# Performance work log

Measured on AMD Instinct MI355X. Metric: run time of the kernel, lower is better.

Reference implementation:

```python
import jax, jax.numpy as jnp
import numpy as np

HEADS = 8
RATIO = 8
EPS = 1e-5


def conv3d(x, w, b, groups=1, pad=0):
    # x: [N,C,D,H,W], w: [O, C//groups, kd,kh,kw]
    out = jax.lax.conv_general_dilated(
        x, w, window_strides=(1, 1, 1),
        padding=[(pad, pad)] * 3,
        feature_group_count=groups,
        dimension_numbers=('NCDHW', 'OIDHW', 'NCDHW'))
    return out + b[None, :, None, None, None]


def setup_inputs() -> dict:
    key = jax.random.key(0)
    ks = jax.random.split(key, 8)
    n, C, t, h, w = 4, 512, 16, 28, 28
    Cm = C // RATIO           # 64
    Kc, Vc = 256, 256
    s = 0.05
    return {
        'x': jax.random.normal(ks[0], (n, C, t, h, w), jnp.float32),
        'pw1_w': jax.random.normal(ks[1], (Cm, C, 1, 1, 1), jnp.float32) * s,
        'pw1_b': jnp.zeros((Cm,), jnp.float32),
        'dw_w': jax.random.normal(ks[2], (Cm, 1, 3, 3, 3), jnp.float32) * s,
        'dw_b': jnp.zeros((Cm,), jnp.float32),
        'k_w': jax.random.normal(ks[3], (Kc, Cm, 1, 1, 1), jnp.float32) * s,
        'k_b': jnp.zeros((Kc,), jnp.float32),
        'q_w': jax.random.normal(ks[4], (Kc, Cm, 1, 1, 1), jnp.float32) * s,
        'q_b': jnp.zeros((Kc,), jnp.float32),
        'v_w': jax.random.normal(ks[5], (Vc, Cm, 1, 1, 1), jnp.float32) * s,
        'v_b': jnp.zeros((Vc,), jnp.float32),
        'rp_w': jax.random.normal(ks[6], (C, Vc, 1, 1, 1), jnp.float32) * s,
        'rp_b': jnp.zeros((C,), jnp.float32),
    }


def reference(x, pw1_w, pw1_b, dw_w, dw_b, k_w, k_b, q_w, q_b, v_w, v_b, rp_w, rp_b):
    n, C, t, h, w = x.shape
    N = t * h * w
    Cm = pw1_w.shape[0]
    Kc, Vc = k_w.shape[0], v_w.shape[0]
    hk, hv = Kc // HEADS, Vc // HEADS

    residual = x
    # DepthwiseConv: 1x1x1 pointwise then 3x3x3 depthwise
    mid = conv3d(x, pw1_w, pw1_b)
    mid = conv3d(mid, dw_w, dw_b, groups=Cm, pad=1)

    keys = conv3d(mid, k_w, k_b).reshape(n, HEADS, hk, N)
    queries = conv3d(mid, q_w, q_b).reshape(n, HEADS, hk, N)
    values = conv3d(mid, v_w, v_b).reshape(n, HEADS, hv, N)

    # linear attention: softmax keys over tokens, queries over head channels
    key = jax.nn.softmax(keys, axis=3)       # over N tokens
    query = jax.nn.softmax(queries, axis=2)  # over hk channels

    # context: [n, H, hk, hv]
    context = jnp.einsum('nhkt,nhvt->nhkv', key, values)
    # attended: [n, H, hv, N]
    attended = jnp.einsum('nhkv,nhkt->nhvt', context, query)
    aggregated = attended.reshape(n, Vc, t, h, w)

    out = conv3d(aggregated, rp_w, rp_b) + residual
    # f.layer_norm(x, x.size()): normalize over the ENTIRE tensor (all dims)
    mu = out.mean()
    var = out.var()
    return (out - mu) / jnp.sqrt(var + EPS)
```

## Files before the change

### kernel.cpp

```cpp
#include <hip/hip_runtime.h>
#include <hip/hip_bf16.h>
#include <math.h>

#define NB 4
#define S_TOK 12544
#define N_TOTAL 25690112ull
#define EPS 1e-5f

typedef short s16x8 __attribute__((ext_vector_type(8)));
typedef float f32x4 __attribute__((ext_vector_type(4)));

__device__ __forceinline__ short f2bf(float f) {
    unsigned u = __builtin_bit_cast(unsigned, f);
    u += 0x7fffu + ((u >> 16) & 1u);
    return (short)(u >> 16);
}

__global__ __launch_bounds__(256) void prep_k(
    const float* __restrict__ pw1_w, const float* __restrict__ k_w,
    const float* __restrict__ q_w, const float* __restrict__ rp_w,
    short* __restrict__ wb)
{
    int i = blockIdx.x * 256 + threadIdx.x;
#pragma unroll
    for (int r = 0; r < 4; ++r, i += 49152) {
        float v;
        if (i < 32768) v = pw1_w[i];
        else if (i < 49152) v = k_w[i - 32768];
        else if (i < 65536) v = q_w[i - 49152];
        else v = rp_w[i - 65536];
        wb[i] = f2bf(v);
    }
}

template<int NT, int WM, int WS, bool XTRANS, bool EPI>
__global__ __launch_bounds__(NT) void gemm_mfma(
    const short* __restrict__ Wb, const float* __restrict__ bias,
    const void* __restrict__ Xv, float* __restrict__ O,
    const float* __restrict__ R, float* __restrict__ stats,
    int M, int K, int S)
{
    constexpr int BM = WM * 64;
    constexpr int BS = WS * 64;
    __shared__ __align__(16) short Xt[BS][64];
    __shared__ __align__(16) short Wt[BM][64];

    const int tid  = threadIdx.x;
    const int lane = tid & 63;
    const int wave = tid >> 6;
    const int mb = blockIdx.x * BM;
    const int sb = blockIdx.y * BS;
    const size_t nb = blockIdx.z;

    const int wm0 = (wave / WS) * 64;
    const int ws0 = (wave % WS) * 64;

    f32x4 acc[4][4];
#pragma unroll
    for (int i = 0; i < 4; ++i)
#pragma unroll
        for (int j = 0; j < 4; ++j) acc[i][j] = (f32x4){0.f, 0.f, 0.f, 0.f};

    const int srow = tid >> 1;
    const int sb4  = (tid & 1) * 4;

    for (int k0 = 0; k0 < K; k0 += 64) {
        __syncthreads();
        {
            const short* wrow = Wb + (size_t)(mb + srow) * K + k0;
            const int sw = srow & 7;
#pragma unroll
            for (int b = 0; b < 4; ++b) {
                const int blk = sb4 + b;
                s16x8 v = *(const s16x8*)(wrow + (blk ^ sw) * 8);
                *(s16x8*)(&Wt[srow][blk * 8]) = v;
            }
        }
        if (XTRANS) {
            const int kr = tid & 63;
            constexpr int SPAN = (BS * 64) / NT;
            const int s0 = (tid >> 6) * SPAN;
            const float* xr = (const float*)Xv + nb * (size_t)K * S
                              + (size_t)(k0 + kr) * S + sb + s0;
            const int blo = (kr & 7) * 2;
            const int bhi = kr >> 3;
            char* base = (char*)Xt;
#pragma unroll
            for (int u = 0; u < SPAN / 4; ++u) {
                float4 v = *(const float4*)(xr + u * 4);
                const int s_ = s0 + u * 4;
                *(short*)(base + (s_ + 0) * 128 + ((bhi ^ ((s_ + 0) & 7)) << 4) + blo) = f2bf(v.x);
                *(short*)(base + (s_ + 1) * 128 + ((bhi ^ ((s_ + 1) & 7)) << 4) + blo) = f2bf(v.y);
                *(short*)(base + (s_ + 2) * 128 + ((bhi ^ ((s_ + 2) & 7)) << 4) + blo) = f2bf(v.z);
                *(short*)(base + (s_ + 3) * 128 + ((bhi ^ ((s_ + 3) & 7)) << 4) + blo) = f2bf(v.w);
            }
        } else {
            const short* xrow = (const short*)Xv + nb * (size_t)S * K
                                + (size_t)(sb + srow) * K + k0;
            const int sw = srow & 7;
#pragma unroll
            for (int b = 0; b < 4; ++b) {
                const int blk = sb4 + b;
                s16x8 v = *(const s16x8*)(xrow + (blk ^ sw) * 8);
                *(s16x8*)(&Xt[srow][blk * 8]) = v;
            }
        }
        __syncthreads();

#pragma unroll
        for (int kk = 0; kk < 2; ++kk) {
            s16x8 af[4], bg[4];
#pragma unroll
            for (int i = 0; i < 4; ++i) {
                const int row = ws0 + i * 16 + (lane & 15);
                const int blk = (kk * 4 + (lane >> 4)) ^ (row & 7);
                af[i] = *(const s16x8*)((const char*)Xt + row * 128 + blk * 16);
            }
#pragma unroll
            for (int j = 0; j < 4; ++j) {
                const int row = wm0 + j * 16 + (lane & 15);
                const int blk = (kk * 4 + (lane >> 4)) ^ (row & 7);
                bg[j] = *(const s16x8*)((const char*)Wt + row * 128 + blk * 16);
            }
#pragma unroll
            for (int i = 0; i < 4; ++i)
#pragma unroll
                for (int j = 0; j < 4; ++j)
                    acc[i][j] = __builtin_amdgcn_mfma_f32_16x16x32_bf16(
                        af[i], bg[j], acc[i][j], 0, 0, 0);
        }
    }

    float lsum = 0.f, lss = 0.f;
    const int chL = lane & 15, tq = (lane >> 4) * 4;
#pragma unroll
    for (int j = 0; j < 4; ++j) {
        const int ch = mb + wm0 + j * 16 + chL;
        const float bi = bias[ch];
        float* orow = O + nb * (size_t)M * S + (size_t)ch * S;
#pragma unroll
        for (int i = 0; i < 4; ++i) {
            const int t0 = sb + ws0 + i * 16 + tq;
            f32x4 a = acc[i][j];
            a.x += bi; a.y += bi; a.z += bi; a.w += bi;
            if (EPI) {
                const float4 r = *(const float4*)(R + nb * (size_t)M * S + (size_t)ch * S + t0);
                a.x += r.x; a.y += r.y; a.z += r.z; a.w += r.w;
                lsum += a.x + a.y + a.z + a.w;
                lss  += a.x * a.x + a.y * a.y + a.z * a.z + a.w * a.w;
            }
            *(f32x4*)(orow + t0) = a;
        }
    }

    if (EPI) {
#pragma unroll
        for (int o = 32; o; o >>= 1) {
            lsum += __shfl_down(lsum, o);
            lss  += __shfl_down(lss, o);
        }
        __shared__ float s1[4], s2[4];
        if (!lane) { s1[wave] = lsum; s2[wave] = lss; }
        __syncthreads();
        if (!tid) {
            atomicAdd(&stats[0], s1[0] + s1[1] + s1[2] + s1[3]);
            atomicAdd(&stats[1], s2[0] + s2[1] + s2[2] + s2[3]);
        }
    }
}

__global__ __launch_bounds__(256) void dw_k(
    const float* __restrict__ in, const float* __restrict__ w,
    const float* __restrict__ b, float* __restrict__ out)
{
    const int idx = blockIdx.x;
    const int d = idx & 15;
    const int c = (idx >> 4) & 63;
    const int n = idx >> 10;

    float wr[27];
#pragma unroll
    for (int i = 0; i < 27; ++i) wr[i] = w[c * 27 + i];
    const float bb = b[c];

    const float* base = in + (size_t)(n * 64 + c) * 16 * 784;
    float* ob = out + ((size_t)(n * 64 + c) * 16 + d) * 784;

    for (int p = threadIdx.x; p < 784; p += 256) {
        const int hh = p / 28, ww = p - hh * 28;
        float acc = bb;
#pragma unroll
        for (int kd = 0; kd < 3; ++kd) {
            const int dd = d + kd - 1;
            if ((unsigned)dd >= 16u) continue;
#pragma unroll
            for (int kh = 0; kh < 3; ++kh) {
                const int h2 = hh + kh - 1;
                if ((unsigned)h2 >= 28u) continue;
#pragma unroll
                for (int kw = 0; kw < 3; ++kw) {
                    const int w2 = ww + kw - 1;
                    if ((unsigned)w2 >= 28u) continue;
                    acc += base[(size_t)dd * 784 + h2 * 28 + w2] * wr[kd * 9 + kh * 3 + kw];
                }
            }
        }
        ob[p] = acc;
    }
}

__global__ __launch_bounds__(256) void kstat_k(
    const float* __restrict__ keys, float* __restrict__ kstats)
{
    const int row = blockIdx.x;
    const float* r = keys + (size_t)row * S_TOK;
    const int tid = threadIdx.x;

    float mx = -INFINITY;
    for (int i = tid; i < S_TOK; i += 256) mx = fmaxf(mx, r[i]);
#pragma unroll
    for (int o = 32; o; o >>= 1) mx = fmaxf(mx, __shfl_down(mx, o));

    __shared__ float sm[4];
    __shared__ float bmx;
    const int lane = tid & 63, wid = tid >> 6;
    if (!lane) sm[wid] = mx;
    __syncthreads();
    if (!tid) bmx = fmaxf(fmaxf(sm[0], sm[1]), fmaxf(sm[2], sm[3]));
    __syncthreads();
    const float M = bmx;

    float s = 0.f;
    for (int i = tid; i < S_TOK; i += 256) s += __expf(r[i] - M);
#pragma unroll
    for (int o = 32; o; o >>= 1) s += __shfl_down(s, o);
    __shared__ float ss[4];
    if (!lane) ss[wid] = s;
    __syncthreads();
    if (!tid) {
        kstats[row * 2]     = M;
        kstats[row * 2 + 1] = ss[0] + ss[1] + ss[2] + ss[3];
    }
}

__global__ __launch_bounds__(256) void km_k(
    const float* __restrict__ keys, const float* __restrict__ kstats,
    const float* __restrict__ mid, float* __restrict__ kmp)
{
    __shared__ float Ke[32][68];
    __shared__ float Mi[64][68];

    const int nh = blockIdx.x;
    const int p  = blockIdx.y;
    const int n  = nh >> 3;
    const int tid = threadIdx.x;

    const int lr = tid >> 3;
    const int lt = (tid & 7) * 8;
    const int rowg = n * 256 + (nh & 7) * 32 + lr;
    const float mx = kstats[rowg * 2];
    const float* krow = keys + (size_t)rowg * S_TOK;

    const int mc = tid & 63;
    const int mq = (tid >> 6) * 16;
    const float* mrow = mid + (size_t)(n * 64 + mc) * S_TOK;

    const int k  = tid & 31;
    const int c0 = (tid >> 5) * 8;

    float acc[8] = {};

    for (int tile = 0; tile < 4; ++tile) {
        const int tb = p * 256 + tile * 64;
        __syncthreads();
        {
            float4 a  = *(const float4*)&krow[tb + lt];
            float4 b4 = *(const float4*)&krow[tb + lt + 4];
            Ke[lr][lt + 0] = __expf(a.x - mx);
            Ke[lr][lt + 1] = __expf(a.y - mx);
            Ke[lr][lt + 2] = __expf(a.z - mx);
            Ke[lr][lt + 3] = __expf(a.w - mx);
            Ke[lr][lt + 4] = __expf(b4.x - mx);
            Ke[lr][lt + 5] = __expf(b4.y - mx);
            Ke[lr][lt + 6] = __expf(b4.z - mx);
            Ke[lr][lt + 7] = __expf(b4.w - mx);
#pragma unroll
            for (int u = 0; u < 4; ++u)
                *(float4*)&Mi[mc][mq + u * 4] = *(const float4*)&mrow[tb + mq + u * 4];
        }
        __syncthreads();
#pragma unroll
        for (int tt = 0; tt < 64; tt += 16) {
            float ke[16];
#pragma unroll
            for (int u = 0; u < 4; ++u)
                *(float4*)&ke[u * 4] = *(const float4*)&Ke[k][tt + u * 4];
#pragma unroll
            for (int j = 0; j < 8; ++j) {
                const float* mr = &Mi[c0 + j][tt];
#pragma unroll
                for (int u = 0; u < 4; ++u) {
                    const float4 m4 = *(const float4*)&mr[u * 4];
                    acc[j] += ke[u * 4 + 0] * m4.x + ke[u * 4 + 1] * m4.y
                            + ke[u * 4 + 2] * m4.z + ke[u * 4 + 3] * m4.w;
                }
            }
        }
    }

    float* outp = kmp + (((size_t)p * 32 + nh) * 32 + k) * 64 + c0;
#pragma unroll
    for (int j = 0; j < 8; ++j) outp[j] = acc[j];
}

__global__ __launch_bounds__(1024) void ctx_k(
    const float* __restrict__ kmp, const float* __restrict__ kstats,
    const float* __restrict__ vw, const float* __restrict__ vb,
    float* __restrict__ ctx)
{
    __shared__ float KM[32][64];
    const int nh = blockIdx.x;
    const int n = nh >> 3;
    const int tid = threadIdx.x;

    for (int e = tid; e < 2048; e += 1024) {
        const int k = e >> 6, c = e & 63;
        float s = 0.f;
        for (int p = 0; p < 49; ++p)
            s += kmp[(((size_t)p * 32 + nh) * 32 + k) * 64 + c];
        const float sum = kstats[(n * 256 + (nh & 7) * 32 + k) * 2 + 1];
        KM[k][c] = s / sum;
    }
    __syncthreads();

    const int k = tid >> 5, v = tid & 31;
    const int hv = (nh & 7) * 32 + v;
    float acc = vb[hv];
#pragma unroll
    for (int c = 0; c < 64; ++c) acc += KM[k][c] * vw[hv * 64 + c];
    ctx[((size_t)nh * 32 + k) * 32 + v] = acc;
}

__global__ __launch_bounds__(256) void attn_k(
    const float* __restrict__ q, const float* __restrict__ ctx,
    short* __restrict__ aggT)
{
    __shared__ float Cl[32][32];
    const int n = blockIdx.z, h = blockIdx.y;
    const int t = blockIdx.x * 256 + threadIdx.x;
    const int nh = n * 8 + h;

    for (int e = threadIdx.x; e < 1024; e += 256)
        Cl[e >> 5][e & 31] = ctx[(size_t)nh * 1024 + e];
    __syncthreads();

    float qs[32];
    const float* qb = q + ((size_t)n * 256 + h * 32) * S_TOK + t;
    float mx = -INFINITY;
#pragma unroll
    for (int k = 0; k < 32; ++k) {
        qs[k] = qb[(size_t)k * S_TOK];
        mx = fmaxf(mx, qs[k]);
    }
    float s = 0.f;
#pragma unroll
    for (int k = 0; k < 32; ++k) {
        qs[k] = __expf(qs[k] - mx);
        s += qs[k];
    }
    const float inv = 1.0f / s;

    short* ab = aggT + ((size_t)n * S_TOK + t) * 256 + h * 32;
#pragma unroll
    for (int u = 0; u < 4; ++u) {
        s16x8 o;
#pragma unroll
        for (int e = 0; e < 8; ++e) {
            const int v = u * 8 + e;
            float a = 0.f;
#pragma unroll
            for (int k = 0; k < 32; ++k) a += Cl[k][v] * qs[k];
            o[e] = f2bf(a * inv);
        }
        *(s16x8*)(ab + u * 8) = o;
    }
}

__global__ __launch_bounds__(256) void ln_k(
    float* __restrict__ O, const float* __restrict__ stats, size_t n4)
{
    const float NT = (float)N_TOTAL;
    const float mu = stats[0] / NT;
    const float var = stats[1] / NT - mu * mu;
    const float inv = rsqrtf(var + EPS);
    float4* p = (float4*)O;
    for (size_t i = (size_t)blockIdx.x * blockDim.x + threadIdx.x; i < n4;
         i += (size_t)gridDim.x * blockDim.x) {
        float4 v = p[i];
        v.x = (v.x - mu) * inv;
        v.y = (v.y - mu) * inv;
        v.z = (v.z - mu) * inv;
        v.w = (v.w - mu) * inv;
        p[i] = v;
    }
}

extern "C" void kernel_launch(void* const* d_in, const int* in_sizes, int n_in,
                              void* d_out, int out_size, void* d_ws, size_t ws_size,
                              hipStream_t stream)
{
    const float* x     = (const float*)d_in[0];
    const float* pw1_w = (const float*)d_in[1];
    const float* pw1_b = (const float*)d_in[2];
    const float* dw_w  = (const float*)d_in[3];
    const float* dw_b  = (const float*)d_in[4];
    const float* k_w   = (const float*)d_in[5];
    const float* k_b   = (const float*)d_in[6];
    const float* q_w   = (const float*)d_in[7];
    const float* q_b   = (const float*)d_in[8];
    const float* v_w   = (const float*)d_in[9];
    const float* v_b   = (const float*)d_in[10];
    const float* rp_w  = (const float*)d_in[11];
    const float* rp_b  = (const float*)d_in[12];
    float* out = (float*)d_out;

    float* ws      = (float*)d_ws;
    float* lnstats = ws;
    float* kstats  = ws + 16;
    float* ctx     = kstats + 2048;
    float* kmp     = ctx + 32768;
    float* mid0    = kmp + 3211264;
    float* mid     = mid0 + 3211264;
    float* kq      = mid + 3211264;
    short* aggT    = (short*)(kq + 12845056);
    short* wb      = (short*)(kq + 12845056 + 6422528);

    hipMemsetAsync(lnstats, 0, 2 * sizeof(float), stream);

    const dim3 b256(256);

    prep_k<<<dim3(192), b256, 0, stream>>>(pw1_w, k_w, q_w, rp_w, wb);
    gemm_mfma<128, 1, 2, true, false><<<dim3(1, 98, NB), dim3(128), 0, stream>>>(
        wb, pw1_b, x, mid0, nullptr, nullptr, 64, 512, S_TOK);
    dw_k<<<dim3(4096), b256, 0, stream>>>(mid0, dw_w, dw_b, mid);
    gemm_mfma<256, 2, 2, true, false><<<dim3(2, 98, NB), b256, 0, stream>>>(
        wb + 32768, k_b, mid, kq, nullptr, nullptr, 256, 64, S_TOK);
    kstat_k<<<dim3(1024), b256, 0, stream>>>(kq, kstats);
    km_k<<<dim3(32, 49), b256, 0, stream>>>(kq, kstats, mid, kmp);
    ctx_k<<<dim3(32), dim3(1024), 0, stream>>>(kmp, kstats, v_w, v_b, ctx);
    gemm_mfma<256, 2, 2, true, false><<<dim3(2, 98, NB), b256, 0, stream>>>(
        wb + 49152, q_b, mid, kq, nullptr, nullptr, 256, 64, S_TOK);
    attn_k<<<dim3(49, 8, NB), b256, 0, stream>>>(kq, ctx, aggT);
    gemm_mfma<256, 2, 2, false, true><<<dim3(4, 98, NB), b256, 0, stream>>>(
        wb + 65536, rp_b, aggT, out, x, lnstats, 512, 256, S_TOK);
    ln_k<<<dim3(2048), b256, 0, stream>>>(out, lnstats, N_TOTAL / 4);
}
```

Baseline: 550.7 us.

## Merge K/Q projection into bf16 GEMM, MFMA key-context, split-K pointwise conv

The K and Q projections now run as a single 512-row GEMM that writes bf16, with the key softmax statistics folded into a new MFMA-based km_k. That kernel exponentiates keys without max subtraction and emits per-chunk exp sums, which removes the separate kstat pass. The first pointwise GEMM uses split-K with two partial outputs, which the depthwise kernel sums; that kernel also writes a bf16 copy of its output for km_k. The final projection GEMM loads its bf16 tiles with global_load_lds direct-to-LDS transfers. Together these cut fp32 traffic and kernel count, but dropping the max shift risks exp overflow for large key values and adds bf16 rounding.

```diff
diff --git a/kernel.cpp b/kernel.cpp
--- a/kernel.cpp
+++ b/kernel.cpp
@@ -8,6 +8,7 @@
 #define EPS 1e-5f
 
 typedef short s16x8 __attribute__((ext_vector_type(8)));
+typedef short s16x4 __attribute__((ext_vector_type(4)));
 typedef float f32x4 __attribute__((ext_vector_type(4)));
 
 __device__ __forceinline__ short f2bf(float f) {
@@ -15,13 +16,19 @@
     u += 0x7fffu + ((u >> 16) & 1u);
     return (short)(u >> 16);
 }
+__device__ __forceinline__ float bf2f(short s) {
+    return __builtin_bit_cast(float, ((unsigned)(unsigned short)s) << 16);
+}
 
 __global__ __launch_bounds__(256) void prep_k(
     const float* __restrict__ pw1_w, const float* __restrict__ k_w,
     const float* __restrict__ q_w, const float* __restrict__ rp_w,
-    short* __restrict__ wb)
-{
-    int i = blockIdx.x * 256 + threadIdx.x;
+    const float* __restrict__ k_b, const float* __restrict__ q_b,
+    short* __restrict__ wb, float* __restrict__ biaskq)
+{
+    int g = blockIdx.x * 256 + threadIdx.x;
+    if (g < 512) biaskq[g] = g < 256 ? k_b[g] : q_b[g - 256];
+    int i = g;
 #pragma unroll
     for (int r = 0; r < 4; ++r, i += 49152) {
         float v;
@@ -33,10 +40,10 @@
     }
 }
 
-template<int NT, int WM, int WS, bool XTRANS, bool EPI>
+template<int NT, int WM, int WS, bool XTRANS, bool GLD, bool OUTBF16, bool EPI, int KSPLIT>
 __global__ __launch_bounds__(NT) void gemm_mfma(
     const short* __restrict__ Wb, const float* __restrict__ bias,
-    const void* __restrict__ Xv, float* __restrict__ O,
+    const void* __restrict__ Xv, void* __restrict__ Ov,
     const float* __restrict__ R, float* __restrict__ stats,
     int M, int K, int S)
 {
@@ -48,8 +55,9 @@
     const int tid  = threadIdx.x;
     const int lane = tid & 63;
     const int wave = tid >> 6;
-    const int mb = blockIdx.x * BM;
-    const int sb = blockIdx.y * BS;
+    const int kc   = (KSPLIT > 1) ? (int)(blockIdx.x % KSPLIT) : 0;
+    const int mb   = ((KSPLIT > 1) ? (int)(blockIdx.x / KSPLIT) : (int)blockIdx.x) * BM;
+    const int sb   = blockIdx.y * BS;
     const size_t nb = blockIdx.z;
 
     const int wm0 = (wave / WS) * 64;
@@ -61,48 +69,59 @@
 #pragma unroll
         for (int j = 0; j < 4; ++j) acc[i][j] = (f32x4){0.f, 0.f, 0.f, 0.f};
 
+    const int kLen = K / KSPLIT;
+    const int kBeg = kc * kLen;
     const int srow = tid >> 1;
     const int sb4  = (tid & 1) * 4;
 
-    for (int k0 = 0; k0 < K; k0 += 64) {
+    for (int k0 = kBeg; k0 < kBeg + kLen; k0 += 64) {
         __syncthreads();
-        {
-            const short* wrow = Wb + (size_t)(mb + srow) * K + k0;
-            const int sw = srow & 7;
-#pragma unroll
-            for (int b = 0; b < 4; ++b) {
-                const int blk = sb4 + b;
-                s16x8 v = *(const s16x8*)(wrow + (blk ^ sw) * 8);
-                *(s16x8*)(&Wt[srow][blk * 8]) = v;
-            }
-        }
-        if (XTRANS) {
-            const int kr = tid & 63;
-            constexpr int SPAN = (BS * 64) / NT;
-            const int s0 = (tid >> 6) * SPAN;
-            const float* xr = (const float*)Xv + nb * (size_t)K * S
-                              + (size_t)(k0 + kr) * S + sb + s0;
-            const int blo = (kr & 7) * 2;
-            const int bhi = kr >> 3;
-            char* base = (char*)Xt;
-#pragma unroll
-            for (int u = 0; u < SPAN / 4; ++u) {
-                float4 v = *(const float4*)(xr + u * 4);
-                const int s_ = s0 + u * 4;
-                *(short*)(base + (s_ + 0) * 128 + ((bhi ^ ((s_ + 0) & 7)) << 4) + blo) = f2bf(v.x);
-                *(short*)(base + (s_ + 1) * 128 + ((bhi ^ ((s_ + 1) & 7)) << 4) + blo) = f2bf(v.y);
-                *(short*)(base + (s_ + 2) * 128 + ((bhi ^ ((s_ + 2) & 7)) << 4) + blo) = f2bf(v.z);
-                *(short*)(base + (s_ + 3) * 128 + ((bhi ^ ((s_ + 3) & 7)) << 4) + blo) = f2bf(v.w);
+        if constexpr (GLD) {
+            const int u0 = wave * 4;
+#pragma unroll
+            for (int u = 0; u < 4; ++u) {
+                const int r = (u0 + u) * 8 + (lane >> 3);
+                const int blkS = ((lane & 7) ^ (r & 7)) * 8;
+                const short* wsrc = Wb + (size_t)(mb + r) * K + k0 + blkS;
+                __builtin_amdgcn_global_load_lds(
+                    (const __attribute__((address_space(1))) unsigned*)wsrc,
+                    (__attribute__((address_space(3))) unsigned*)((char*)Wt + (u0 + u) * 1024),
+                    16, 0, 0);
+                const short* xsrc = (const short*)Xv + (nb * (size_t)S + sb + r) * K + k0 + blkS;
+                __builtin_amdgcn_global_load_lds(
+                    (const __attribute__((address_space(1))) unsigned*)xsrc,
+                    (__attribute__((address_space(3))) unsigned*)((char*)Xt + (u0 + u) * 1024),
+                    16, 0, 0);
             }
         } else {
-            const short* xrow = (const short*)Xv + nb * (size_t)S * K
-                                + (size_t)(sb + srow) * K + k0;
-            const int sw = srow & 7;
-#pragma unroll
-            for (int b = 0; b < 4; ++b) {
-                const int blk = sb4 + b;
-                s16x8 v = *(const s16x8*)(xrow + (blk ^ sw) * 8);
-                *(s16x8*)(&Xt[srow][blk * 8]) = v;
+            {
+                const short* wrow = Wb + (size_t)(mb + srow) * K + k0;
+                const int sw = srow & 7;
+#pragma unroll
+                for (int b = 0; b < 4; ++b) {
+                    const int blk = sb4 + b;
+                    s16x8 v = *(const s16x8*)(wrow + ((blk ^ sw) * 8));
+                    *(s16x8*)(&Wt[srow][blk * 8]) = v;
+                }
+            }
+            if constexpr (XTRANS) {
+                const int kr = tid & 63;
+                constexpr int SPAN = (BS * 64) / NT;
+                const int s0 = (tid >> 6) * SPAN;
+                const float* xr = (const float*)Xv + nb * (size_t)K * S
+                                  + (size_t)(k0 + kr) * S + sb + s0;
+                const int blo = (kr & 7) * 2;
+                const int bhi = kr >> 3;
+                char* base = (char*)Xt;
+#pragma unroll
+                for (int u = 0; u < SPAN / 4; ++u) {
+                    float4 v = *(const float4*)(xr + u * 4);
+                    const int s_ = s0 + u * 4;
+                    *(short*)(base + (s_ + 0) * 128 + ((bhi ^ ((s_ + 0) & 7)) << 4) + blo) = f2bf(v.x);
+                    *(short*)(base + (s_ + 1) * 128 + ((bhi ^ ((s_ + 1) & 7)) << 4) + blo) = f2bf(v.y);
+                    *(short*)(base + (s_ + 2) * 128 + ((bhi ^ ((s_ + 2) & 7)) << 4) + blo) = f2bf(v.z);
+                    *(short*)(base + (s_ + 3) * 128 + ((bhi ^ ((s_ + 3) & 7)) << 4) + blo) = f2bf(v.w);
+                }
             }
         }
         __syncthreads();
@@ -136,24 +155,36 @@
 #pragma unroll
     for (int j = 0; j < 4; ++j) {
         const int ch = mb + wm0 + j * 16 + chL;
-        const float bi = bias[ch];
-        float* orow = O + nb * (size_t)M * S + (size_t)ch * S;
-#pragma unroll
-        for (int i = 0; i < 4; ++i) {
-            const int t0 = sb + ws0 + i * 16 + tq;
-            f32x4 a = acc[i][j];
-            a.x += bi; a.y += bi; a.z += bi; a.w += bi;
-            if (EPI) {
-                const float4 r = *(const float4*)(R + nb * (size_t)M * S + (size_t)ch * S + t0);
-                a.x += r.x; a.y += r.y; a.z += r.z; a.w += r.w;
-                lsum += a.x + a.y + a.z + a.w;
-                lss  += a.x * a.x + a.y * a.y + a.z * a.z + a.w * a.w;
-            }
-            *(f32x4*)(orow + t0) = a;
-        }
-    }
-
-    if (EPI) {
+        const float bi = (kc == 0) ? bias[ch] : 0.f;
+        if constexpr (OUTBF16) {
+            short* Ob = (short*)Ov + nb * (size_t)M * S + (size_t)ch * S;
+#pragma unroll
+            for (int i = 0; i < 4; ++i) {
+                const int t0 = sb + ws0 + i * 16 + tq;
+                f32x4 a = acc[i][j];
+                s16x4 o = (s16x4){f2bf(a.x + bi), f2bf(a.y + bi), f2bf(a.z + bi), f2bf(a.w + bi)};
+                *(s16x4*)(Ob + t0) = o;
+            }
+        } else {
+            float* Ob = (float*)Ov + ((KSPLIT > 1) ? (size_t)kc * NB * M * S : 0)
+                        + nb * (size_t)M * S + (size_t)ch * S;
+#pragma unroll
+            for (int i = 0; i < 4; ++i) {
+                const int t0 = sb + ws0 + i * 16 + tq;
+                f32x4 a = acc[i][j];
+                a.x += bi; a.y += bi; a.z += bi; a.w += bi;
+                if constexpr (EPI) {
+                    const float4 r = *(const float4*)(R + nb * (size_t)M * S + (size_t)ch * S + t0);
+                    a.x += r.x; a.y += r.y; a.z += r.z; a.w += r.w;
+                    lsum += a.x + a.y + a.z + a.w;
+                    lss  += a.x * a.x + a.y * a.y + a.z * a.z + a.w * a.w;
+                }
+                *(f32x4*)(Ob + t0) = a;
+            }
+        }
+    }
+
+    if constexpr (EPI) {
 #pragma unroll
         for (int o = 32; o; o >>= 1) {
             lsum += __shfl_down(lsum, o);
@@ -170,8 +201,9 @@
 }
 
 __global__ __launch_bounds__(256) void dw_k(
-    const float* __restrict__ in, const float* __restrict__ w,
-    const float* __restrict__ b, float* __restrict__ out)
+    const float* __restrict__ p0, const float* __restrict__ w,
+    const float* __restrict__ b, float* __restrict__ out,
+    short* __restrict__ outb)
 {
     const int idx = blockIdx.x;
     const int d = idx & 15;
@@ -183,8 +215,12 @@
     for (int i = 0; i < 27; ++i) wr[i] = w[c * 27 + i];
     const float bb = b[c];
 
-    const float* base = in + (size_t)(n * 64 + c) * 16 * 784;
-    float* ob = out + ((size_t)(n * 64 + c) * 16 + d) * 784;
+    const size_t slab = (size_t)(n * 64 + c) * 16 * 784;
+    const float* b0 = p0 + slab;
+    const float* b1 = p0 + 3211264 + slab;
+    const size_t obase = ((size_t)(n * 64 + c) * 16 + d) * 784;
+    float* ob = out + obase;
+    short* obb = outb + obase;
 
     for (int p = threadIdx.x; p < 784; p += 256) {
         const int hh = p / 28, ww = p - hh * 28;
@@ -201,135 +237,109 @@
                 for (int kw = 0; kw < 3; ++kw) {
                     const int w2 = ww + kw - 1;
                     if ((unsigned)w2 >= 28u) continue;
-                    acc += base[(size_t)dd * 784 + h2 * 28 + w2] * wr[kd * 9 + kh * 3 + kw];
+                    const size_t off = (size_t)dd * 784 + h2 * 28 + w2;
+                    acc += (b0[off] + b1[off]) * wr[kd * 9 + kh * 3 + kw];
                 }
             }
         }
         ob[p] = acc;
-    }
-}
-
-__global__ __launch_bounds__(256) void kstat_k(
-    const float* __restrict__ keys, float* __restrict__ kstats)
-{
-    const int row = blockIdx.x;
-    const float* r = keys + (size_t)row * S_TOK;
-    const int tid = threadIdx.x;
-
-    float mx = -INFINITY;
-    for (int i = tid; i < S_TOK; i += 256) mx = fmaxf(mx, r[i]);
-#pragma unroll
-    for (int o = 32; o; o >>= 1) mx = fmaxf(mx, __shfl_down(mx, o));
-
-    __shared__ float sm[4];
-    __shared__ float bmx;
-    const int lane = tid & 63, wid = tid >> 6;
-    if (!lane) sm[wid] = mx;
-    __syncthreads();
-    if (!tid) bmx = fmaxf(fmaxf(sm[0], sm[1]), fmaxf(sm[2], sm[3]));
-    __syncthreads();
-    const float M = bmx;
-
-    float s = 0.f;
-    for (int i = tid; i < S_TOK; i += 256) s += __expf(r[i] - M);
-#pragma unroll
-    for (int o = 32; o; o >>= 1) s += __shfl_down(s, o);
-    __shared__ float ss[4];
-    if (!lane) ss[wid] = s;
-    __syncthreads();
-    if (!tid) {
-        kstats[row * 2]     = M;
-        kstats[row * 2 + 1] = ss[0] + ss[1] + ss[2] + ss[3];
+        obb[p] = f2bf(acc);
     }
 }
 
 __global__ __launch_bounds__(256) void km_k(
-    const float* __restrict__ keys, const float* __restrict__ kstats,
-    const float* __restrict__ mid, float* __restrict__ kmp)
-{
-    __shared__ float Ke[32][68];
-    __shared__ float Mi[64][68];
-
-    const int nh = blockIdx.x;
-    const int p  = blockIdx.y;
-    const int n  = nh >> 3;
-    const int tid = threadIdx.x;
-
-    const int lr = tid >> 3;
-    const int lt = (tid & 7) * 8;
-    const int rowg = n * 256 + (nh & 7) * 32 + lr;
-    const float mx = kstats[rowg * 2];
-    const float* krow = keys + (size_t)rowg * S_TOK;
-
-    const int mc = tid & 63;
-    const int mq = (tid >> 6) * 16;
-    const float* mrow = mid + (size_t)(n * 64 + mc) * S_TOK;
-
-    const int k  = tid & 31;
-    const int c0 = (tid >> 5) * 8;
-
-    float acc[8] = {};
-
-    for (int tile = 0; tile < 4; ++tile) {
-        const int tb = p * 256 + tile * 64;
-        __syncthreads();
-        {
-            float4 a  = *(const float4*)&krow[tb + lt];
-            float4 b4 = *(const float4*)&krow[tb + lt + 4];
-            Ke[lr][lt + 0] = __expf(a.x - mx);
-            Ke[lr][lt + 1] = __expf(a.y - mx);
-            Ke[lr][lt + 2] = __expf(a.z - mx);
-            Ke[lr][lt + 3] = __expf(a.w - mx);
-            Ke[lr][lt + 4] = __expf(b4.x - mx);
-            Ke[lr][lt + 5] = __expf(b4.y - mx);
-            Ke[lr][lt + 6] = __expf(b4.z - mx);
-            Ke[lr][lt + 7] = __expf(b4.w - mx);
-#pragma unroll
-            for (int u = 0; u < 4; ++u)
-                *(float4*)&Mi[mc][mq + u * 4] = *(const float4*)&mrow[tb + mq + u * 4];
-        }
-        __syncthreads();
-#pragma unroll
-        for (int tt = 0; tt < 64; tt += 16) {
-            float ke[16];
-#pragma unroll
-            for (int u = 0; u < 4; ++u)
-                *(float4*)&ke[u * 4] = *(const float4*)&Ke[k][tt + u * 4];
-#pragma unroll
-            for (int j = 0; j < 8; ++j) {
-                const float* mr = &Mi[c0 + j][tt];
-#pragma unroll
-                for (int u = 0; u < 4; ++u) {
-                    const float4 m4 = *(const float4*)&mr[u * 4];
-                    acc[j] += ke[u * 4 + 0] * m4.x + ke[u * 4 + 1] * m4.y
-                            + ke[u * 4 + 2] * m4.z + ke[u * 4 + 3] * m4.w;
-                }
-            }
-        }
-    }
-
-    float* outp = kmp + (((size_t)p * 32 + nh) * 32 + k) * 64 + c0;
-#pragma unroll
-    for (int j = 0; j < 8; ++j) outp[j] = acc[j];
+    const short* __restrict__ kqb, const short* __restrict__ midb,
+    float* __restrict__ kmp, float* __restrict__ sep)
+{
+    const int chunk = blockIdx.x;
+    const int wave = threadIdx.x >> 6;
+    const int lane = threadIdx.x & 63;
+    const int nh = blockIdx.y * 4 + wave;
+    const int n = nh >> 3, h = nh & 7;
+
+    const int row = lane & 15;
+    const int t0base = chunk * 256 + (lane >> 4) * 8;
+
+    const short* kbase = kqb + ((size_t)n * 512 + h * 32) * S_TOK;
+    const short* mbase = midb + (size_t)n * 64 * S_TOK;
+
+    f32x4 acc[2][4];
+#pragma unroll
+    for (int i = 0; i < 2; ++i)
+#pragma unroll
+        for (int j = 0; j < 4; ++j) acc[i][j] = (f32x4){0.f, 0.f, 0.f, 0.f};
+    float se[2] = {0.f, 0.f};
+
+#pragma unroll
+    for (int st = 0; st < 8; ++st) {
+        const int t0 = t0base + st * 32;
+        s16x8 a[2];
+#pragma unroll
+        for (int i = 0; i < 2; ++i) {
+            s16x8 kv = *(const s16x8*)(kbase + (size_t)(i * 16 + row) * S_TOK + t0);
+            s16x8 e;
+#pragma unroll
+            for (int q = 0; q < 8; ++q) {
+                const float f = __expf(bf2f(kv[q]));
+                se[i] += f;
+                e[q] = f2bf(f);
+            }
+            a[i] = e;
+        }
+#pragma unroll
+        for (int j = 0; j < 4; ++j) {
+            const s16x8 bfr = *(const s16x8*)(mbase + (size_t)(j * 16 + row) * S_TOK + t0);
+#pragma unroll
+            for (int i = 0; i < 2; ++i)
+                acc[i][j] = __builtin_amdgcn_mfma_f32_16x16x32_bf16(a[i], bfr, acc[i][j], 0, 0, 0);
+        }
+    }
+
+#pragma unroll
+    for (int i = 0; i < 2; ++i) {
+        se[i] += __shfl_xor(se[i], 16);
+        se[i] += __shfl_xor(se[i], 32);
+    }
+    if (lane < 16) {
+        sep[((size_t)chunk * 32 + nh) * 32 + row] = se[0];
+        sep[((size_t)chunk * 32 + nh) * 32 + 16 + row] = se[1];
+    }
+
+    float* kp = kmp + ((size_t)chunk * 32 + nh) * 2048;
+#pragma unroll
+    for (int i = 0; i < 2; ++i)
+#pragma unroll
+        for (int j = 0; j < 4; ++j)
+#pragma unroll
+            for (int r = 0; r < 4; ++r) {
+                const int k = i * 16 + (lane >> 4) * 4 + r;
+                kp[k * 64 + j * 16 + row] = acc[i][j][r];
+            }
 }
 
 __global__ __launch_bounds__(1024) void ctx_k(
-    const float* __restrict__ kmp, const float* __restrict__ kstats,
+    const float* __restrict__ kmp, const float* __restrict__ sep,
     const float* __restrict__ vw, const float* __restrict__ vb,
     float* __restrict__ ctx)
 {
     __shared__ float KM[32][64];
+    __shared__ float ses[32];
     const int nh = blockIdx.x;
-    const int n = nh >> 3;
     const int tid = threadIdx.x;
+
+    if (tid < 32) {
+        float s = 0.f;
+        for (int p = 0; p < 49; ++p) s += sep[((size_t)p * 32 + nh) * 32 + tid];
+        ses[tid] = s;
+    }
+    __syncthreads();
 
     for (int e = tid; e < 2048; e += 1024) {
         const int k = e >> 6, c = e & 63;
         float s = 0.f;
         for (int p = 0; p < 49; ++p)
-            s += kmp[(((size_t)p * 32 + nh) * 32 + k) * 64 + c];
-        const float sum = kstats[(n * 256 + (nh & 7) * 32 + k) * 2 + 1];
-        KM[k][c] = s / sum;
+            s += kmp[((size_t)p * 32 + nh) * 2048 + e];
+        KM[k][c] = s / ses[k];
     }
     __syncthreads();
 
@@ -342,7 +352,7 @@
 }
 
 __global__ __launch_bounds__(256) void attn_k(
-    const float* __restrict__ q, const float* __restrict__ ctx,
+    const short* __restrict__ kqb, const float* __restrict__ ctx,
     short* __restrict__ aggT)
 {
     __shared__ float Cl[32][32];
@@ -355,11 +365,11 @@
     __syncthreads();
 
     float qs[32];
-    const float* qb = q + ((size_t)n * 256 + h * 32) * S_TOK + t;
+    const short* qb = kqb + ((size_t)n * 512 + 256 + h * 32) * S_TOK + t;
     float mx = -INFINITY;
 #pragma unroll
     for (int k = 0; k < 32; ++k) {
-        qs[k] = qb[(size_t)k * S_TOK];
+        qs[k] = bf2f(qb[(size_t)k * S_TOK]);
         mx = fmaxf(mx, qs[k]);
     }
     float s = 0.f;
@@ -426,32 +436,31 @@
 
     float* ws      = (float*)d_ws;
     float* lnstats = ws;
-    float* kstats  = ws + 16;
-    float* ctx     = kstats + 2048;
-    float* kmp     = ctx + 32768;
-    float* mid0    = kmp + 3211264;
-    float* mid     = mid0 + 3211264;
-    float* kq      = mid + 3211264;
-    short* aggT    = (short*)(kq + 12845056);
-    short* wb      = (short*)(kq + 12845056 + 6422528);
+    float* biaskq  = ws + 16;
+    float* sep     = ws + 528;
+    float* ctx     = ws + 50704;
+    float* kmp     = ws + 83472;
+    float* mid0p   = ws + 3294736;
+    float* mid     = ws + 9717264;
+    short* midb    = (short*)(ws + 12928528);
+    short* kqb     = (short*)(ws + 14534160);
+    short* aggT    = (short*)(ws + 27379216);
+    short* wb      = (short*)(ws + 33801744);
 
     hipMemsetAsync(lnstats, 0, 2 * sizeof(float), stream);
 
     const dim3 b256(256);
 
-    prep_k<<<dim3(192), b256, 0, stream>>>(pw1_w, k_w, q_w, rp_w, wb);
-    gemm_mfma<128, 1, 2, true, false><<<dim3(1, 98, NB), dim3(128), 0, stream>>>(
-        wb, pw1_b, x, mid0, nullptr, nullptr, 64, 512, S_TOK);
-    dw_k<<<dim3(4096), b256, 0, stream>>>(mid0, dw_w, dw_b, mid);
-    gemm_mfma<256, 2, 2, true, false><<<dim3(2, 98, NB), b256, 0, stream>>>(
-        wb + 32768, k_b, mid, kq, nullptr, nullptr, 256, 64, S_TOK);
-    kstat_k<<<dim3(1024), b256, 0, stream>>>(kq, kstats);
-    km_k<<<dim3(32, 49), b256, 0, stream>>>(kq, kstats, mid, kmp);
-    ctx_k<<<dim3(32), dim3(1024), 0, stream>>>(kmp, kstats, v_w, v_b, ctx);
-    gemm_mfma<256, 2, 2, true, false><<<dim3(2, 98, NB), b256, 0, stream>>>(
-        wb + 49152, q_b, mid, kq, nullptr, nullptr, 256, 64, S_TOK);
-    attn_k<<<dim3(49, 8, NB), b256, 0, stream>>>(kq, ctx, aggT);
-    gemm_mfma<256, 2, 2, false, true><<<dim3(4, 98, NB), b256, 0, stream>>>(
+    prep_k<<<dim3(192), b256, 0, stream>>>(pw1_w, k_w, q_w, rp_w, k_b, q_b, wb, biaskq);
+    gemm_mfma<128, 1, 2, true, false, false, false, 2><<<dim3(2, 98, NB), dim3(128), 0, stream>>>(
+        wb, pw1_b, x, mid0p, nullptr, nullptr, 64, 512, S_TOK);
+    dw_k<<<dim3(4096), b256, 0, stream>>>(mid0p, dw_w, dw_b, mid, midb);
+    gemm_mfma<256, 2, 2, true, false, true, false, 1><<<dim3(4, 98, NB), b256, 0, stream>>>(
+        wb + 32768, biaskq, mid, kqb, nullptr, nullptr, 512, 64, S_TOK);
+    km_k<<<dim3(49, 8), b256, 0, stream>>>(kqb, midb, kmp, sep);
+    ctx_k<<<dim3(32), dim3(1024), 0, stream>>>(kmp, sep, v_w, v_b, ctx);
+    attn_k<<<dim3(49, 8, NB), b256, 0, stream>>>(kqb, ctx, aggT);
+    gemm_mfma<256, 2, 2, false, true, false, true, 1><<<dim3(4, 98, NB), b256, 0, stream>>>(
         wb + 65536, rp_b, aggT, out, x, lnstats, 512, 256, S_TOK);
     ln_k<<<dim3(2048), b256, 0, stream>>>(out, lnstats, N_TOTAL / 4);
 }
```

After: 463.8 us. 1.19x faster.
